# Kernel optimization log

Hardware: AMD Instinct MI355X
Metric: run time of the kernel (lower is better)

## Reference

```python
import jax, jax.numpy as jnp
import numpy as np

BN_EPS = 1e-5
N_OUT, D_OUT = 64, 128


def setup_inputs() -> dict:
    key = jax.random.key(0)
    k1, k2, k3, k4 = jax.random.split(key, 4)
    B, N_in, D_in, K = 512, 64, 128, 4
    x = jax.random.normal(k1, (B, N_in, D_in), dtype=jnp.float32)
    # block-sparse weights: one (D_in x D_out) block per (output-row, active-input-row) pair
    W = jax.random.normal(k2, (N_OUT, K, D_in, D_OUT), dtype=jnp.float32) * (1.0 / np.sqrt(K * D_in))
    bias = jax.random.normal(k3, (N_OUT, D_OUT), dtype=jnp.float32) * 0.02
    gamma = jnp.ones((N_OUT * D_OUT,), dtype=jnp.float32)
    beta = jnp.zeros((N_OUT * D_OUT,), dtype=jnp.float32)
    idx = jax.random.randint(k4, (N_OUT, K), 0, N_in, dtype=jnp.int32)
    return {"x": x, "W": W, "bias": bias, "gamma": gamma, "beta": beta, "idx": idx}


def reference(x, W, bias, gamma, beta, idx):
    B = x.shape[0]
    # structured-sparse linear: gather active input rows, per-block matmul
    xg = x[:, idx, :]                                   # [B, N_out, K, D_in]
    y = jnp.einsum('bokd,okde->boe', xg, W) + bias      # [B, N_out, D_out]
    # BatchNorm1d (training-mode batch statistics) on flattened features
    yf = y.reshape(B, -1)                               # [B, N_out*D_out]
    mean = jnp.mean(yf, axis=0)
    var = jnp.mean(jnp.square(yf - mean), axis=0)       # biased variance, as in torch BN
    yn = (yf - mean) * jax.lax.rsqrt(var + BN_EPS) * gamma + beta
    # Swish: z * sigmoid(z)
    out = yn * jax.nn.sigmoid(yn)
    return out.reshape(B, N_OUT, D_OUT)
```

## Files before the change

kernel.cpp:

```cpp
#include <hip/hip_runtime.h>


typedef __attribute__((ext_vector_type(8))) __bf16 bf16x8;
typedef __attribute__((ext_vector_type(4))) __bf16 bf16x4;
typedef __attribute__((ext_vector_type(4))) float  f32x4;

#define B_SZ   512
#define N_IN   64
#define D_IN   128
#define N_O    64
#define D_O    128
#define FEAT   (N_O * D_O)
#define LDA    40

__global__ __launch_bounds__(256, 2)
void gemm_stats_kernel(const float* __restrict__ x, const float* __restrict__ W,
                       const float* __restrict__ bias, const int* __restrict__ idxp,
                       __bf16* __restrict__ y, float* __restrict__ psum,
                       float* __restrict__ psq)
{
    __shared__ __bf16 Alds[128 * LDA];
    __shared__ __bf16 Blds[128 * LDA];

    const int bx   = blockIdx.x;
    const int o    = bx >> 2;
    const int bt   = bx & 3;
    const int b0   = bt * 128;
    const int tid  = threadIdx.x;
    const int wave = tid >> 6;
    const int lane = tid & 63;
    const int wr   = wave >> 1;
    const int wc   = wave & 1;
    const int lam  = lane & 15;
    const int quad = lane >> 4;

    int rsel[4];
#pragma unroll
    for (int k = 0; k < 4; ++k) rsel[k] = idxp[o * 4 + k];

    const f32x4 zero4 = {0.f, 0.f, 0.f, 0.f};
    f32x4 acc[4][4];
#pragma unroll
    for (int mi = 0; mi < 4; ++mi)
#pragma unroll
        for (int ni = 0; ni < 4; ++ni) acc[mi][ni] = zero4;

    const int m_a = tid >> 1;
    const int ca  = (tid & 1) * 16;

    for (int kk = 0; kk < 16; ++kk) {
        const int kidx = kk >> 2;
        const int d0   = (kk & 3) * 32;
        const int r    = rsel[kidx];

        const float* xa = x + (((b0 + m_a) * N_IN + r) * D_IN + d0 + ca);
        f32x4 xv0 = *(const f32x4*)(xa + 0);
        f32x4 xv1 = *(const f32x4*)(xa + 4);
        f32x4 xv2 = *(const f32x4*)(xa + 8);
        f32x4 xv3 = *(const f32x4*)(xa + 12);
        bf16x8 p0, p1;
        p0[0] = (__bf16)xv0[0]; p0[1] = (__bf16)xv0[1];
        p0[2] = (__bf16)xv0[2]; p0[3] = (__bf16)xv0[3];
        p0[4] = (__bf16)xv1[0]; p0[5] = (__bf16)xv1[1];
        p0[6] = (__bf16)xv1[2]; p0[7] = (__bf16)xv1[3];
        p1[0] = (__bf16)xv2[0]; p1[1] = (__bf16)xv2[1];
        p1[2] = (__bf16)xv2[2]; p1[3] = (__bf16)xv2[3];
        p1[4] = (__bf16)xv3[0]; p1[5] = (__bf16)xv3[1];
        p1[6] = (__bf16)xv3[2]; p1[7] = (__bf16)xv3[3];

        bf16x4 wb[4];
        int te[4], tdg[4];
#pragma unroll
        for (int it = 0; it < 4; ++it) {
            const int task = it * 256 + tid;
            const int e  = task & 127;
            const int dg = task >> 7;
            te[it] = e; tdg[it] = dg;
            const float* wp = W + (((o * 4 + kidx) * 128 + (d0 + dg * 4)) * 128 + e);
            wb[it][0] = (__bf16)wp[0];
            wb[it][1] = (__bf16)wp[128];
            wb[it][2] = (__bf16)wp[256];
            wb[it][3] = (__bf16)wp[384];
        }

        __syncthreads();
        *(bf16x8*)&Alds[m_a * LDA + ca]     = p0;
        *(bf16x8*)&Alds[m_a * LDA + ca + 8] = p1;
#pragma unroll
        for (int it = 0; it < 4; ++it)
            *(bf16x4*)&Blds[te[it] * LDA + tdg[it] * 4] = wb[it];
        __syncthreads();

        bf16x8 af[4], bfv[4];
#pragma unroll
        for (int mi = 0; mi < 4; ++mi)
            af[mi] = *(const bf16x8*)&Alds[(wr * 64 + mi * 16 + lam) * LDA + quad * 8];
#pragma unroll
        for (int ni = 0; ni < 4; ++ni)
            bfv[ni] = *(const bf16x8*)&Blds[(wc * 64 + ni * 16 + lam) * LDA + quad * 8];
#pragma unroll
        for (int mi = 0; mi < 4; ++mi)
#pragma unroll
            for (int ni = 0; ni < 4; ++ni)
                acc[mi][ni] = __builtin_amdgcn_mfma_f32_16x16x32_bf16(
                    af[mi], bfv[ni], acc[mi][ni], 0, 0, 0);
    }

    const int nbase = wc * 64;
    float bvals[4];
#pragma unroll
    for (int ni = 0; ni < 4; ++ni)
        bvals[ni] = bias[o * 128 + nbase + ni * 16 + lam];

#pragma unroll
    for (int mi = 0; mi < 4; ++mi)
#pragma unroll
        for (int ni = 0; ni < 4; ++ni)
#pragma unroll
            for (int rr = 0; rr < 4; ++rr) acc[mi][ni][rr] += bvals[ni];

#pragma unroll
    for (int mi = 0; mi < 4; ++mi) {
        const int mrow = b0 + wr * 64 + mi * 16 + quad * 4;
#pragma unroll
        for (int ni = 0; ni < 4; ++ni) {
            const int col = o * 128 + nbase + ni * 16 + lam;
#pragma unroll
            for (int rr = 0; rr < 4; ++rr)
                y[(mrow + rr) * FEAT + col] = (__bf16)acc[mi][ni][rr];
        }
    }

#pragma unroll
    for (int ni = 0; ni < 4; ++ni) {
        float s = 0.f, q = 0.f;
#pragma unroll
        for (int mi = 0; mi < 4; ++mi)
#pragma unroll
            for (int rr = 0; rr < 4; ++rr) {
                const float v = acc[mi][ni][rr];
                s += v; q += v * v;
            }
        s += __shfl_xor(s, 16); s += __shfl_xor(s, 32);
        q += __shfl_xor(q, 16); q += __shfl_xor(q, 32);
        if (quad == 0) {
            const int slot = bt * 2 + wr;
            const int e    = nbase + ni * 16 + lam;
            psum[(o * 8 + slot) * 128 + e] = s;
            psq [(o * 8 + slot) * 128 + e] = q;
        }
    }
}

__global__ __launch_bounds__(256, 4)
void norm_silu_kernel(const __bf16* __restrict__ y, const float* __restrict__ psum,
                      const float* __restrict__ psq, const float* __restrict__ gamma,
                      const float* __restrict__ beta, float* __restrict__ out)
{
    __shared__ float sscale[128];
    __shared__ float sshift[128];
    const int o   = blockIdx.x >> 3;
    const int bc  = blockIdx.x & 7;
    const int tid = threadIdx.x;

    if (tid < 128) {
        float s = 0.f, q = 0.f;
#pragma unroll
        for (int sl = 0; sl < 8; ++sl) {
            s += psum[(o * 8 + sl) * 128 + tid];
            q += psq [(o * 8 + sl) * 128 + tid];
        }
        const float mean = s * (1.0f / 512.0f);
        const float var  = q * (1.0f / 512.0f) - mean * mean;
        const float rstd = rsqrtf(var + 1e-5f);
        const float sc   = rstd * gamma[o * 128 + tid];
        sscale[tid] = sc;
        sshift[tid] = beta[o * 128 + tid] - mean * sc;
    }
    __syncthreads();

#pragma unroll
    for (int it = 0; it < 8; ++it) {
        const int lin = it * 1024 + tid * 4;
        const int bl  = lin >> 7;
        const int e   = lin & 127;
        const int g   = (bc * 64 + bl) * FEAT + o * 128 + e;
        bf16x4 y4 = *(const bf16x4*)&y[g];
        f32x4 ov;
#pragma unroll
        for (int j = 0; j < 4; ++j) {
            const float v  = (float)y4[j];
            const float xn = v * sscale[e + j] + sshift[e + j];
            const float sg = 1.0f / (1.0f + __expf(-xn));
            ov[j] = xn * sg;
        }
        *(f32x4*)&out[g] = ov;
    }
}

extern "C" void kernel_launch(void* const* d_in, const int* in_sizes, int n_in,
                              void* d_out, int out_size, void* d_ws, size_t ws_size,
                              hipStream_t stream)
{
    const float* x     = (const float*)d_in[0];
    const float* W     = (const float*)d_in[1];
    const float* bias  = (const float*)d_in[2];
    const float* gamma = (const float*)d_in[3];
    const float* beta  = (const float*)d_in[4];
    const int*   idx   = (const int*)d_in[5];
    float* out = (float*)d_out;

    __bf16* y   = (__bf16*)d_ws;
    float* psum = (float*)((char*)d_ws + (size_t)B_SZ * FEAT * sizeof(__bf16));
    float* psq  = psum + 64 * 8 * 128;

    gemm_stats_kernel<<<dim3(256), dim3(256), 0, stream>>>(x, W, bias, idx, y, psum, psq);
    norm_silu_kernel<<<dim3(512), dim3(256), 0, stream>>>(y, psum, psq, gamma, beta, out);
}
```

Before: 107.0 us.

## Fuse GEMM, batch-norm statistics and Swish into one kernel per output row

Merges the GEMM+stats kernel and the normalize+Swish kernel into a single kernel where each 1024-thread block owns one output row across the whole batch. Batch statistics are reduced in shared memory and applied directly to the accumulators, so the bf16 intermediate y and the partial-sum buffers are no longer written to or read from global memory, and one launch is removed. In exchange, the grid shrinks to 64 blocks, leaving most compute units idle. Each block also runs the full K loop on a larger tile, and output stores become narrower.

New measurement: 121.9 us. +13.9%, slower.

```diff
diff --git a/kernel.cpp b/kernel.cpp
--- a/kernel.cpp
+++ b/kernel.cpp
@@ -13,19 +13,20 @@
 #define FEAT   (N_O * D_O)
 #define LDA    40
 
-__global__ __launch_bounds__(256, 2)
-void gemm_stats_kernel(const float* __restrict__ x, const float* __restrict__ W,
-                       const float* __restrict__ bias, const int* __restrict__ idxp,
-                       __bf16* __restrict__ y, float* __restrict__ psum,
-                       float* __restrict__ psq)
+__global__ __launch_bounds__(1024, 4)
+void fused_encoder_kernel(const float* __restrict__ x, const float* __restrict__ W,
+                          const float* __restrict__ bias, const float* __restrict__ gamma,
+                          const float* __restrict__ beta, const int* __restrict__ idxp,
+                          float* __restrict__ out)
 {
-    __shared__ __bf16 Alds[128 * LDA];
+    __shared__ __bf16 Alds[512 * LDA];
     __shared__ __bf16 Blds[128 * LDA];
+    __shared__ float  Sred[8 * 128];
+    __shared__ float  Qred[8 * 128];
+    __shared__ float  sscale[128];
+    __shared__ float  sshift[128];
 
-    const int bx   = blockIdx.x;
-    const int o    = bx >> 2;
-    const int bt   = bx & 3;
-    const int b0   = bt * 128;
+    const int o    = blockIdx.x;
     const int tid  = threadIdx.x;
     const int wave = tid >> 6;
     const int lane = tid & 63;
@@ -47,13 +48,15 @@
 
     const int m_a = tid >> 1;
     const int ca  = (tid & 1) * 16;
+    const int e_b = tid & 127;
+    const int dgb = tid >> 7;
 
     for (int kk = 0; kk < 16; ++kk) {
         const int kidx = kk >> 2;
         const int d0   = (kk & 3) * 32;
         const int r    = rsel[kidx];
 
-        const float* xa = x + (((b0 + m_a) * N_IN + r) * D_IN + d0 + ca);
+        const float* xa = x + ((m_a * N_IN + r) * D_IN + d0 + ca);
         f32x4 xv0 = *(const f32x4*)(xa + 0);
         f32x4 xv1 = *(const f32x4*)(xa + 4);
         f32x4 xv2 = *(const f32x4*)(xa + 8);
@@ -68,27 +71,17 @@
         p1[4] = (__bf16)xv3[0]; p1[5] = (__bf16)xv3[1];
         p1[6] = (__bf16)xv3[2]; p1[7] = (__bf16)xv3[3];
 
-        bf16x4 wb[4];
-        int te[4], tdg[4];
-#pragma unroll
-        for (int it = 0; it < 4; ++it) {
-            const int task = it * 256 + tid;
-            const int e  = task & 127;
-            const int dg = task >> 7;
-            te[it] = e; tdg[it] = dg;
-            const float* wp = W + (((o * 4 + kidx) * 128 + (d0 + dg * 4)) * 128 + e);
-            wb[it][0] = (__bf16)wp[0];
-            wb[it][1] = (__bf16)wp[128];
-            wb[it][2] = (__bf16)wp[256];
-            wb[it][3] = (__bf16)wp[384];
-        }
+        const float* wp = W + (((o * 4 + kidx) * 128 + (d0 + dgb * 4)) * 128 + e_b);
+        bf16x4 wb;
+        wb[0] = (__bf16)wp[0];
+        wb[1] = (__bf16)wp[128];
+        wb[2] = (__bf16)wp[256];
+        wb[3] = (__bf16)wp[384];
 
         __syncthreads();
         *(bf16x8*)&Alds[m_a * LDA + ca]     = p0;
         *(bf16x8*)&Alds[m_a * LDA + ca + 8] = p1;
-#pragma unroll
-        for (int it = 0; it < 4; ++it)
-            *(bf16x4*)&Blds[te[it] * LDA + tdg[it] * 4] = wb[it];
+        *(bf16x4*)&Blds[e_b * LDA + dgb * 4] = wb;
         __syncthreads();
 
         bf16x8 af[4], bfv[4];
@@ -111,25 +104,12 @@
 #pragma unroll
     for (int ni = 0; ni < 4; ++ni)
         bvals[ni] = bias[o * 128 + nbase + ni * 16 + lam];
-
 #pragma unroll
     for (int mi = 0; mi < 4; ++mi)
 #pragma unroll
         for (int ni = 0; ni < 4; ++ni)
 #pragma unroll
             for (int rr = 0; rr < 4; ++rr) acc[mi][ni][rr] += bvals[ni];
-
-#pragma unroll
-    for (int mi = 0; mi < 4; ++mi) {
-        const int mrow = b0 + wr * 64 + mi * 16 + quad * 4;
-#pragma unroll
-        for (int ni = 0; ni < 4; ++ni) {
-            const int col = o * 128 + nbase + ni * 16 + lam;
-#pragma unroll
-            for (int rr = 0; rr < 4; ++rr)
-                y[(mrow + rr) * FEAT + col] = (__bf16)acc[mi][ni][rr];
-        }
-    }
 
 #pragma unroll
     for (int ni = 0; ni < 4; ++ni) {
@@ -144,31 +124,19 @@
         s += __shfl_xor(s, 16); s += __shfl_xor(s, 32);
         q += __shfl_xor(q, 16); q += __shfl_xor(q, 32);
         if (quad == 0) {
-            const int slot = bt * 2 + wr;
-            const int e    = nbase + ni * 16 + lam;
-            psum[(o * 8 + slot) * 128 + e] = s;
-            psq [(o * 8 + slot) * 128 + e] = q;
+            const int e = nbase + ni * 16 + lam;
+            Sred[wr * 128 + e] = s;
+            Qred[wr * 128 + e] = q;
         }
     }
-}
-
-__global__ __launch_bounds__(256, 4)
-void norm_silu_kernel(const __bf16* __restrict__ y, const float* __restrict__ psum,
-                      const float* __restrict__ psq, const float* __restrict__ gamma,
-                      const float* __restrict__ beta, float* __restrict__ out)
-{
-    __shared__ float sscale[128];
-    __shared__ float sshift[128];
-    const int o   = blockIdx.x >> 3;
-    const int bc  = blockIdx.x & 7;
-    const int tid = threadIdx.x;
+    __syncthreads();
 
     if (tid < 128) {
         float s = 0.f, q = 0.f;
 #pragma unroll
         for (int sl = 0; sl < 8; ++sl) {
-            s += psum[(o * 8 + sl) * 128 + tid];
-            q += psq [(o * 8 + sl) * 128 + tid];
+            s += Sred[sl * 128 + tid];
+            q += Qred[sl * 128 + tid];
         }
         const float mean = s * (1.0f / 512.0f);
         const float var  = q * (1.0f / 512.0f) - mean * mean;
@@ -180,21 +148,20 @@
     __syncthreads();
 
 #pragma unroll
-    for (int it = 0; it < 8; ++it) {
-        const int lin = it * 1024 + tid * 4;
-        const int bl  = lin >> 7;
-        const int e   = lin & 127;
-        const int g   = (bc * 64 + bl) * FEAT + o * 128 + e;
-        bf16x4 y4 = *(const bf16x4*)&y[g];
-        f32x4 ov;
+    for (int mi = 0; mi < 4; ++mi) {
+        const int rowb = wr * 64 + mi * 16 + quad * 4;
 #pragma unroll
-        for (int j = 0; j < 4; ++j) {
-            const float v  = (float)y4[j];
-            const float xn = v * sscale[e + j] + sshift[e + j];
-            const float sg = 1.0f / (1.0f + __expf(-xn));
-            ov[j] = xn * sg;
+        for (int ni = 0; ni < 4; ++ni) {
+            const int col = nbase + ni * 16 + lam;
+            const float sc = sscale[col];
+            const float sh = sshift[col];
+#pragma unroll
+            for (int rr = 0; rr < 4; ++rr) {
+                const float xn = acc[mi][ni][rr] * sc + sh;
+                const float sg = 1.0f / (1.0f + __expf(-xn));
+                out[(rowb + rr) * FEAT + o * 128 + col] = xn * sg;
+            }
         }
-        *(f32x4*)&out[g] = ov;
     }
 }
 
@@ -210,10 +177,6 @@
     const int*   idx   = (const int*)d_in[5];
     float* out = (float*)d_out;
 
-    __bf16* y   = (__bf16*)d_ws;
-    float* psum = (float*)((char*)d_ws + (size_t)B_SZ * FEAT * sizeof(__bf16));
-    float* psq  = psum + 64 * 8 * 128;
-
-    gemm_stats_kernel<<<dim3(256), dim3(256), 0, stream>>>(x, W, bias, idx, y, psum, psq);
-    norm_silu_kernel<<<dim3(512), dim3(256), 0, stream>>>(y, psum, psq, gamma, beta, out);
+    fused_encoder_kernel<<<dim3(64), dim3(1024), 0, stream>>>(
+        x, W, bias, gamma, beta, idx, out);
 }
```
